# Performance work log

Hardware: AMD Instinct MI355X
Metric: run time of the kernel (lower is better)

The kernel has to match this reference:

```python
import jax, jax.numpy as jnp
import numpy as np

N_NODES = 40000
N_EDGES = 640000
D = 128  # in_channels == out_channels (required by the module's math)


def setup_inputs() -> dict:
    key = jax.random.key(0)
    ks = jax.random.split(key, 8)
    s = 1.0 / np.sqrt(D)  # torch Linear default init scale
    x = jax.random.normal(ks[0], (N_NODES, D), dtype=jnp.float32)
    edge_index = jax.random.randint(ks[1], (2, N_EDGES), 0, N_NODES, dtype=jnp.int64)
    Wn_w = jax.random.uniform(ks[2], (D, D), jnp.float32, -s, s)
    Wn_b = jax.random.uniform(ks[3], (D,), jnp.float32, -s, s)
    Wg_w = jax.random.uniform(ks[4], (D, D), jnp.float32, -s, s)
    Wg_b = jax.random.uniform(ks[5], (D,), jnp.float32, -s, s)
    Wa_w = jax.random.uniform(ks[6], (D, D), jnp.float32, -s, s)
    Wa_b = jax.random.uniform(ks[7], (D,), jnp.float32, -s, s)
    return {"x": x, "edge_index": edge_index,
            "Wn_w": Wn_w, "Wn_b": Wn_b,
            "Wg_w": Wg_w, "Wg_b": Wg_b,
            "Wa_w": Wa_w, "Wa_b": Wa_b}


def reference(x, edge_index, Wn_w, Wn_b, Wg_w, Wg_b, Wa_w, Wa_b):
    row, col = edge_index[0], edge_index[1]
    x_col = x[col]                                  # [E, D] gather
    alpha = jax.nn.sigmoid(x_col @ Wa_w + Wa_b)     # [E, D] edge attention
    neigh = x_col * alpha                           # [E, D]
    aggr = jax.ops.segment_sum(neigh, row, num_segments=x.shape[0])  # [N, D]
    out = jnp.tanh((x @ Wn_w + Wn_b) + (aggr @ Wg_w + Wg_b))
    return out  # dropout p=0.0 is identity
```

## Files before the change

### kernel.cpp

```cpp
#include <hip/hip_runtime.h>

#define NN 40000
#define NE 640000
#define D 128
#define CAP 64

typedef __attribute__((ext_vector_type(8))) short short8;
typedef __attribute__((ext_vector_type(4))) float f32x4;
typedef __attribute__((ext_vector_type(4))) int i32x4;

__device__ __forceinline__ short f2b(float v) {
  unsigned int u = __builtin_bit_cast(unsigned int, v);
  u = (u + 0x7fffu + ((u >> 16) & 1u)) >> 16;
  return (short)u;
}
__device__ __forceinline__ float b2f(short s) {
  unsigned int u = ((unsigned int)(unsigned short)s) << 16;
  return __builtin_bit_cast(float, u);
}

__global__ __launch_bounds__(256) void k_prep(
    const float* __restrict__ Wn, const float* __restrict__ Wg,
    const float* __restrict__ Wa, short* __restrict__ WnT,
    short* __restrict__ WgThi, short* __restrict__ WgTlo,
    short* __restrict__ WaT, int* __restrict__ cnt) {
  int i = blockIdx.x * 256 + threadIdx.x;
  int k = i >> 7, c = i & 127;
  WnT[c * D + k] = f2b(Wn[k * D + c]);
  WaT[c * D + k] = f2b(Wa[k * D + c]);
  float v = Wg[k * D + c];
  short hi = f2b(v);
  WgThi[c * D + k] = hi;
  WgTlo[c * D + k] = f2b(v - b2f(hi));
  if (i < 10000) {
    i32x4 z = {0, 0, 0, 0};
    *(i32x4*)(cnt + i * 4) = z;
  }
}

__global__ __launch_bounds__(256) void k_node(
    const float* __restrict__ x, const short* __restrict__ WaT,
    const short* __restrict__ WnT, const float* __restrict__ ba,
    float* __restrict__ xn_out, short* __restrict__ h_out) {
  int r0 = blockIdx.x * 16;
  int w = threadIdx.x >> 6, l = threadIdx.x & 63;
  int g = l >> 4, c16 = l & 15;
  int rowA = r0 + c16;

  short8 a[4];
#pragma unroll
  for (int kt = 0; kt < 4; ++kt) {
    const float* p = x + (size_t)rowA * D + kt * 32 + g * 8;
    f32x4 v0 = *(const f32x4*)p;
    f32x4 v1 = *(const f32x4*)(p + 4);
    short8 t;
    t[0] = f2b(v0[0]); t[1] = f2b(v0[1]); t[2] = f2b(v0[2]); t[3] = f2b(v0[3]);
    t[4] = f2b(v1[0]); t[5] = f2b(v1[1]); t[6] = f2b(v1[2]); t[7] = f2b(v1[3]);
    a[kt] = t;
  }

#pragma unroll
  for (int u = 0; u < 2; ++u) {
    int ct = w * 2 + u;
    int cc = ct * 16 + c16;
    f32x4 c = {0.f, 0.f, 0.f, 0.f};
#pragma unroll
    for (int kt = 0; kt < 4; ++kt) {
      short8 b = *(const short8*)(WaT + (size_t)cc * D + kt * 32 + g * 8);
      c = __builtin_amdgcn_mfma_f32_16x16x32_bf16(a[kt], b, c, 0, 0, 0);
    }
    float bav = ba[cc];
#pragma unroll
    for (int r = 0; r < 4; ++r) {
      int rr = r0 + g * 4 + r;
      float t = c[r] + bav;
      float al = 1.0f / (1.0f + __expf(-t));
      float xv = x[(size_t)rr * D + cc];
      h_out[(size_t)rr * D + cc] = f2b(xv * al);
    }
    f32x4 cn = {0.f, 0.f, 0.f, 0.f};
#pragma unroll
    for (int kt = 0; kt < 4; ++kt) {
      short8 b = *(const short8*)(WnT + (size_t)cc * D + kt * 32 + g * 8);
      cn = __builtin_amdgcn_mfma_f32_16x16x32_bf16(a[kt], b, cn, 0, 0, 0);
    }
#pragma unroll
    for (int r = 0; r < 4; ++r) {
      int rr = r0 + g * 4 + r;
      xn_out[(size_t)rr * D + cc] = cn[r];
    }
  }
}

__global__ __launch_bounds__(256) void k_fill(
    const int* __restrict__ ei, int* __restrict__ cnt,
    int* __restrict__ bucket) {
  int e = blockIdx.x * 256 + threadIdx.x;
  if (e >= NE) return;
  int r = ei[e];
  int c = ei[NE + e];
  int slot = atomicAdd(&cnt[r], 1);
  if (slot < CAP) bucket[r * CAP + slot] = c;
}

__global__ __launch_bounds__(256) void k_aggr(
    const int* __restrict__ cnt, const int* __restrict__ bucket,
    const short* __restrict__ h, float* __restrict__ s) {
  int l = threadIdx.x & 63;
  int n = blockIdx.x * 4 + (threadIdx.x >> 6);
  if (n >= NN) return;
  int g = l >> 4, i = l & 15;
  int deg = cnt[n];
  deg = deg < CAP ? deg : CAP;
  int bc = bucket[n * CAP + l];
  float acc[8];
#pragma unroll
  for (int q = 0; q < 8; ++q) acc[q] = 0.f;

  int j = 0;
  for (; j + 8 <= deg; j += 8) {
    int c0 = __shfl(bc, j + g);
    int c1 = __shfl(bc, j + 4 + g);
    short8 v0 = *(const short8*)(h + (size_t)c0 * D + i * 8);
    short8 v1 = *(const short8*)(h + (size_t)c1 * D + i * 8);
#pragma unroll
    for (int q = 0; q < 8; ++q) acc[q] += b2f(v0[q]);
#pragma unroll
    for (int q = 0; q < 8; ++q) acc[q] += b2f(v1[q]);
  }
  for (; j < deg; j += 4) {
    int src = j + g;
    int clamped = src < deg ? src : deg - 1;
    int c0 = __shfl(bc, clamped);
    if (src < deg) {
      short8 v0 = *(const short8*)(h + (size_t)c0 * D + i * 8);
#pragma unroll
      for (int q = 0; q < 8; ++q) acc[q] += b2f(v0[q]);
    }
  }

#pragma unroll
  for (int q = 0; q < 8; ++q) {
    acc[q] += __shfl_xor(acc[q], 16);
    acc[q] += __shfl_xor(acc[q], 32);
  }
  if (g == 0) {
    f32x4 lo = {acc[0], acc[1], acc[2], acc[3]};
    f32x4 hi = {acc[4], acc[5], acc[6], acc[7]};
    *(f32x4*)(s + (size_t)n * D + i * 8) = lo;
    *(f32x4*)(s + (size_t)n * D + i * 8 + 4) = hi;
  }
}

__global__ __launch_bounds__(256) void k_final(
    const float* __restrict__ s, const short* __restrict__ WgThi,
    const short* __restrict__ WgTlo, const float* __restrict__ bn,
    const float* __restrict__ bg, float* __restrict__ out) {
  int r0 = blockIdx.x * 16;
  int w = threadIdx.x >> 6, l = threadIdx.x & 63;
  int g = l >> 4, c16 = l & 15;
  int rowA = r0 + c16;

  short8 ahi[4], alo[4];
#pragma unroll
  for (int kt = 0; kt < 4; ++kt) {
    const float* p = s + (size_t)rowA * D + kt * 32 + g * 8;
    f32x4 v0 = *(const f32x4*)p;
    f32x4 v1 = *(const f32x4*)(p + 4);
    short8 hi, lo;
#pragma unroll
    for (int jq = 0; jq < 4; ++jq) {
      short hh = f2b(v0[jq]);
      hi[jq] = hh;
      lo[jq] = f2b(v0[jq] - b2f(hh));
    }
#pragma unroll
    for (int jq = 0; jq < 4; ++jq) {
      short hh = f2b(v1[jq]);
      hi[4 + jq] = hh;
      lo[4 + jq] = f2b(v1[jq] - b2f(hh));
    }
    ahi[kt] = hi;
    alo[kt] = lo;
  }

#pragma unroll
  for (int u = 0; u < 2; ++u) {
    int ct = w * 2 + u;
    int cc = ct * 16 + c16;
    f32x4 c = {0.f, 0.f, 0.f, 0.f};
#pragma unroll
    for (int kt = 0; kt < 4; ++kt) {
      short8 bh = *(const short8*)(WgThi + (size_t)cc * D + kt * 32 + g * 8);
      short8 bl = *(const short8*)(WgTlo + (size_t)cc * D + kt * 32 + g * 8);
      c = __builtin_amdgcn_mfma_f32_16x16x32_bf16(ahi[kt], bh, c, 0, 0, 0);
      c = __builtin_amdgcn_mfma_f32_16x16x32_bf16(alo[kt], bh, c, 0, 0, 0);
      c = __builtin_amdgcn_mfma_f32_16x16x32_bf16(ahi[kt], bl, c, 0, 0, 0);
    }
    float bias = bn[cc] + bg[cc];
#pragma unroll
    for (int r = 0; r < 4; ++r) {
      int rr = r0 + g * 4 + r;
      float z = c[r] + out[(size_t)rr * D + cc] + bias;
      out[(size_t)rr * D + cc] = tanhf(z);
    }
  }
}

extern "C" void kernel_launch(void* const* d_in, const int* in_sizes, int n_in,
                              void* d_out, int out_size, void* d_ws,
                              size_t ws_size, hipStream_t stream) {
  const float* x = (const float*)d_in[0];
  const int* ei = (const int*)d_in[1];
  const float* Wn_w = (const float*)d_in[2];
  const float* Wn_b = (const float*)d_in[3];
  const float* Wg_w = (const float*)d_in[4];
  const float* Wg_b = (const float*)d_in[5];
  const float* Wa_w = (const float*)d_in[6];
  const float* Wa_b = (const float*)d_in[7];

  char* ws = (char*)d_ws;
  short* WaT = (short*)(ws + 0);
  short* WnT = (short*)(ws + 32 * 1024);
  short* WgThi = (short*)(ws + 64 * 1024);
  short* WgTlo = (short*)(ws + 96 * 1024);
  int* cnt = (int*)(ws + 128 * 1024);
  float* s = (float*)(ws + 512 * 1024);
  short* h = (short*)(ws + 512 * 1024 + (size_t)NN * D * 4);
  int* bucket = (int*)(ws + 512 * 1024 + (size_t)NN * D * 6);
  float* out = (float*)d_out;

  k_prep<<<64, 256, 0, stream>>>(Wn_w, Wg_w, Wa_w, WnT, WgThi, WgTlo, WaT, cnt);
  k_node<<<NN / 16, 256, 0, stream>>>(x, WaT, WnT, Wa_b, out, h);
  k_fill<<<(NE + 255) / 256, 256, 0, stream>>>(ei, cnt, bucket);
  k_aggr<<<NN / 4, 256, 0, stream>>>(cnt, bucket, h, s);
  k_final<<<NN / 16, 256, 0, stream>>>(s, WgThi, WgTlo, Wn_b, Wg_b, out);
}
```

Before: 126.4 us.

## Move node linear into final kernel, stage tiles in LDS, compress bucket indices

The x@Wn product moves from k_node into k_final, so the intermediate fp32 result is no longer written to out and read back. k_node and k_final now stage x and s tiles through shared memory for coalesced loads, and h is written as vectorized short8 stores. Bucket indices become 16-bit and a zero sentinel row is added to h, so the aggregation loop runs branch-free in fixed 16-edge steps with padded gathers. The risks are extra redundant sentinel loads for low-degree nodes, and that 16-bit indices only hold because the node count fits in an unsigned short.

Result: faster. 111.3 us (-11.9%).

```diff
diff --git a/kernel.cpp b/kernel.cpp
--- a/kernel.cpp
+++ b/kernel.cpp
@@ -23,7 +23,7 @@
     const float* __restrict__ Wn, const float* __restrict__ Wg,
     const float* __restrict__ Wa, short* __restrict__ WnT,
     short* __restrict__ WgThi, short* __restrict__ WgTlo,
-    short* __restrict__ WaT, int* __restrict__ cnt) {
+    short* __restrict__ WaT, int* __restrict__ cnt, short* __restrict__ h) {
   int i = blockIdx.x * 256 + threadIdx.x;
   int k = i >> 7, c = i & 127;
   WnT[c * D + k] = f2b(Wn[k * D + c]);
@@ -36,75 +36,100 @@
     i32x4 z = {0, 0, 0, 0};
     *(i32x4*)(cnt + i * 4) = z;
   }
-}
-
-__global__ __launch_bounds__(256) void k_node(
-    const float* __restrict__ x, const short* __restrict__ WaT,
-    const short* __restrict__ WnT, const float* __restrict__ ba,
-    float* __restrict__ xn_out, short* __restrict__ h_out) {
-  int r0 = blockIdx.x * 16;
-  int w = threadIdx.x >> 6, l = threadIdx.x & 63;
-  int g = l >> 4, c16 = l & 15;
-  int rowA = r0 + c16;
-
-  short8 a[4];
-#pragma unroll
-  for (int kt = 0; kt < 4; ++kt) {
-    const float* p = x + (size_t)rowA * D + kt * 32 + g * 8;
-    f32x4 v0 = *(const f32x4*)p;
-    f32x4 v1 = *(const f32x4*)(p + 4);
-    short8 t;
-    t[0] = f2b(v0[0]); t[1] = f2b(v0[1]); t[2] = f2b(v0[2]); t[3] = f2b(v0[3]);
-    t[4] = f2b(v1[0]); t[5] = f2b(v1[1]); t[6] = f2b(v1[2]); t[7] = f2b(v1[3]);
-    a[kt] = t;
-  }
-
-#pragma unroll
-  for (int u = 0; u < 2; ++u) {
-    int ct = w * 2 + u;
-    int cc = ct * 16 + c16;
-    f32x4 c = {0.f, 0.f, 0.f, 0.f};
-#pragma unroll
-    for (int kt = 0; kt < 4; ++kt) {
-      short8 b = *(const short8*)(WaT + (size_t)cc * D + kt * 32 + g * 8);
-      c = __builtin_amdgcn_mfma_f32_16x16x32_bf16(a[kt], b, c, 0, 0, 0);
-    }
-    float bav = ba[cc];
-#pragma unroll
-    for (int r = 0; r < 4; ++r) {
-      int rr = r0 + g * 4 + r;
-      float t = c[r] + bav;
-      float al = 1.0f / (1.0f + __expf(-t));
-      float xv = x[(size_t)rr * D + cc];
-      h_out[(size_t)rr * D + cc] = f2b(xv * al);
-    }
-    f32x4 cn = {0.f, 0.f, 0.f, 0.f};
-#pragma unroll
-    for (int kt = 0; kt < 4; ++kt) {
-      short8 b = *(const short8*)(WnT + (size_t)cc * D + kt * 32 + g * 8);
-      cn = __builtin_amdgcn_mfma_f32_16x16x32_bf16(a[kt], b, cn, 0, 0, 0);
-    }
-#pragma unroll
-    for (int r = 0; r < 4; ++r) {
-      int rr = r0 + g * 4 + r;
-      xn_out[(size_t)rr * D + cc] = cn[r];
-    }
+  if (i < 16) {
+    short8 z = {0, 0, 0, 0, 0, 0, 0, 0};
+    *(short8*)(h + (size_t)NN * D + i * 8) = z;
   }
 }
 
 __global__ __launch_bounds__(256) void k_fill(
     const int* __restrict__ ei, int* __restrict__ cnt,
-    int* __restrict__ bucket) {
+    unsigned short* __restrict__ bucket) {
   int e = blockIdx.x * 256 + threadIdx.x;
   if (e >= NE) return;
   int r = ei[e];
   int c = ei[NE + e];
   int slot = atomicAdd(&cnt[r], 1);
-  if (slot < CAP) bucket[r * CAP + slot] = c;
-}
+  if (slot < CAP) bucket[(size_t)r * CAP + slot] = (unsigned short)c;
+}
+
+__global__ __launch_bounds__(256) void k_node(
+    const float* __restrict__ x, const short* __restrict__ WaT,
+    const float* __restrict__ ba, short* __restrict__ h_out) {
+  __shared__ float xs[16][132];
+  __shared__ float al_s[16][132];
+  int r0 = blockIdx.x * 16;
+  int t = threadIdx.x;
+  int w = t >> 6, l = t & 63;
+  int g = l >> 4, c16 = l & 15;
+
+#pragma unroll
+  for (int p = 0; p < 2; ++p) {
+    int idx = t + p * 256;
+    int row = idx >> 5, cv = idx & 31;
+    f32x4 v = *(const f32x4*)(x + (size_t)(r0 + row) * D + cv * 4);
+    *(f32x4*)&xs[row][cv * 4] = v;
+  }
+  __syncthreads();
+
+  short8 a[4];
+#pragma unroll
+  for (int kt = 0; kt < 4; ++kt) {
+    f32x4 v0 = *(const f32x4*)&xs[c16][kt * 32 + g * 8];
+    f32x4 v1 = *(const f32x4*)&xs[c16][kt * 32 + g * 8 + 4];
+    short8 tt;
+    tt[0] = f2b(v0[0]); tt[1] = f2b(v0[1]); tt[2] = f2b(v0[2]); tt[3] = f2b(v0[3]);
+    tt[4] = f2b(v1[0]); tt[5] = f2b(v1[1]); tt[6] = f2b(v1[2]); tt[7] = f2b(v1[3]);
+    a[kt] = tt;
+  }
+
+#pragma unroll
+  for (int u = 0; u < 2; ++u) {
+    int ct = w * 2 + u;
+    int cc = ct * 16 + c16;
+    f32x4 c = {0.f, 0.f, 0.f, 0.f};
+#pragma unroll
+    for (int kt = 0; kt < 4; ++kt) {
+      short8 b = *(const short8*)(WaT + (size_t)cc * D + kt * 32 + g * 8);
+      c = __builtin_amdgcn_mfma_f32_16x16x32_bf16(a[kt], b, c, 0, 0, 0);
+    }
+    float bav = ba[cc];
+#pragma unroll
+    for (int r = 0; r < 4; ++r) {
+      float tv = c[r] + bav;
+      al_s[g * 4 + r][cc] = 1.0f / (1.0f + __expf(-tv));
+    }
+  }
+  __syncthreads();
+
+  short8 hh;
+#pragma unroll
+  for (int q = 0; q < 8; ++q) {
+    float av = al_s[c16][w * 32 + g * 8 + q];
+    float xv = xs[c16][w * 32 + g * 8 + q];
+    hh[q] = f2b(xv * av);
+  }
+  *(short8*)(h_out + (size_t)(r0 + c16) * D + w * 32 + g * 8) = hh;
+}
+
+#define SSTEP(S0, CA, CB, CC, CD)                                   \
+  {                                                                 \
+    int q0 = (S0) + g < deg ? (CA) : NN;                            \
+    int q1 = (S0) + 4 + g < deg ? (CB) : NN;                        \
+    int q2 = (S0) + 8 + g < deg ? (CC) : NN;                        \
+    int q3 = (S0) + 12 + g < deg ? (CD) : NN;                       \
+    short8 v0 = *(const short8*)(h + (size_t)q0 * D + i * 8);       \
+    short8 v1 = *(const short8*)(h + (size_t)q1 * D + i * 8);       \
+    short8 v2 = *(const short8*)(h + (size_t)q2 * D + i * 8);       \
+    short8 v3 = *(const short8*)(h + (size_t)q3 * D + i * 8);       \
+    _Pragma("unroll") for (int q = 0; q < 8; ++q) {                 \
+      acc[q] += b2f(v0[q]) + b2f(v1[q]);                            \
+      acc[q] += b2f(v2[q]) + b2f(v3[q]);                            \
+    }                                                               \
+  }
 
 __global__ __launch_bounds__(256) void k_aggr(
-    const int* __restrict__ cnt, const int* __restrict__ bucket,
+    const int* __restrict__ cnt, const unsigned short* __restrict__ bucket,
     const short* __restrict__ h, float* __restrict__ s) {
   int l = threadIdx.x & 63;
   int n = blockIdx.x * 4 + (threadIdx.x >> 6);
@@ -112,30 +137,24 @@
   int g = l >> 4, i = l & 15;
   int deg = cnt[n];
   deg = deg < CAP ? deg : CAP;
-  int bc = bucket[n * CAP + l];
+  int bc = bucket[(size_t)n * CAP + l];
   float acc[8];
 #pragma unroll
   for (int q = 0; q < 8; ++q) acc[q] = 0.f;
 
-  int j = 0;
-  for (; j + 8 <= deg; j += 8) {
-    int c0 = __shfl(bc, j + g);
-    int c1 = __shfl(bc, j + 4 + g);
-    short8 v0 = *(const short8*)(h + (size_t)c0 * D + i * 8);
-    short8 v1 = *(const short8*)(h + (size_t)c1 * D + i * 8);
-#pragma unroll
-    for (int q = 0; q < 8; ++q) acc[q] += b2f(v0[q]);
-#pragma unroll
-    for (int q = 0; q < 8; ++q) acc[q] += b2f(v1[q]);
-  }
-  for (; j < deg; j += 4) {
-    int src = j + g;
-    int clamped = src < deg ? src : deg - 1;
-    int c0 = __shfl(bc, clamped);
-    if (src < deg) {
-      short8 v0 = *(const short8*)(h + (size_t)c0 * D + i * 8);
-#pragma unroll
-      for (int q = 0; q < 8; ++q) acc[q] += b2f(v0[q]);
+  int c0 = __shfl(bc, g), c1 = __shfl(bc, 4 + g);
+  int c2 = __shfl(bc, 8 + g), c3 = __shfl(bc, 12 + g);
+  SSTEP(0, c0, c1, c2, c3);
+  if (deg > 16) {
+    int c4 = __shfl(bc, 16 + g), c5 = __shfl(bc, 20 + g);
+    int c6 = __shfl(bc, 24 + g), c7 = __shfl(bc, 28 + g);
+    SSTEP(16, c4, c5, c6, c7);
+  }
+  if (deg > 32) {
+    for (int j = 32; j < deg; j += 16) {
+      int d0 = __shfl(bc, (j + g) & 63), d1 = __shfl(bc, (j + 4 + g) & 63);
+      int d2 = __shfl(bc, (j + 8 + g) & 63), d3 = __shfl(bc, (j + 12 + g) & 63);
+      SSTEP(j, d0, d1, d2, d3);
     }
   }
 
@@ -153,35 +172,54 @@
 }
 
 __global__ __launch_bounds__(256) void k_final(
-    const float* __restrict__ s, const short* __restrict__ WgThi,
+    const float* __restrict__ x, const float* __restrict__ s,
+    const short* __restrict__ WnT, const short* __restrict__ WgThi,
     const short* __restrict__ WgTlo, const float* __restrict__ bn,
     const float* __restrict__ bg, float* __restrict__ out) {
+  __shared__ float xs[16][132];
+  __shared__ float ss[16][132];
   int r0 = blockIdx.x * 16;
-  int w = threadIdx.x >> 6, l = threadIdx.x & 63;
+  int t = threadIdx.x;
+  int w = t >> 6, l = t & 63;
   int g = l >> 4, c16 = l & 15;
-  int rowA = r0 + c16;
-
-  short8 ahi[4], alo[4];
+
+#pragma unroll
+  for (int p = 0; p < 2; ++p) {
+    int idx = t + p * 256;
+    int row = idx >> 5, cv = idx & 31;
+    *(f32x4*)&xs[row][cv * 4] =
+        *(const f32x4*)(x + (size_t)(r0 + row) * D + cv * 4);
+    *(f32x4*)&ss[row][cv * 4] =
+        *(const f32x4*)(s + (size_t)(r0 + row) * D + cv * 4);
+  }
+  __syncthreads();
+
+  short8 axf[4], sh[4], sl[4];
 #pragma unroll
   for (int kt = 0; kt < 4; ++kt) {
-    const float* p = s + (size_t)rowA * D + kt * 32 + g * 8;
-    f32x4 v0 = *(const f32x4*)p;
-    f32x4 v1 = *(const f32x4*)(p + 4);
-    short8 hi, lo;
+    f32x4 xv0 = *(const f32x4*)&xs[c16][kt * 32 + g * 8];
+    f32x4 xv1 = *(const f32x4*)&xs[c16][kt * 32 + g * 8 + 4];
+    short8 tx;
+    tx[0] = f2b(xv0[0]); tx[1] = f2b(xv0[1]); tx[2] = f2b(xv0[2]); tx[3] = f2b(xv0[3]);
+    tx[4] = f2b(xv1[0]); tx[5] = f2b(xv1[1]); tx[6] = f2b(xv1[2]); tx[7] = f2b(xv1[3]);
+    axf[kt] = tx;
+    f32x4 sv0 = *(const f32x4*)&ss[c16][kt * 32 + g * 8];
+    f32x4 sv1 = *(const f32x4*)&ss[c16][kt * 32 + g * 8 + 4];
+    short8 th, tl;
 #pragma unroll
     for (int jq = 0; jq < 4; ++jq) {
-      short hh = f2b(v0[jq]);
-      hi[jq] = hh;
-      lo[jq] = f2b(v0[jq] - b2f(hh));
+      short hh = f2b(sv0[jq]);
+      th[jq] = hh;
+      tl[jq] = f2b(sv0[jq] - b2f(hh));
     }
 #pragma unroll
     for (int jq = 0; jq < 4; ++jq) {
-      short hh = f2b(v1[jq]);
-      hi[4 + jq] = hh;
-      lo[4 + jq] = f2b(v1[jq] - b2f(hh));
-    }
-    ahi[kt] = hi;
-    alo[kt] = lo;
+      short hh = f2b(sv1[jq]);
+      th[4 + jq] = hh;
+      tl[4 + jq] = f2b(sv1[jq] - b2f(hh));
+    }
+    sh[kt] = th;
+    sl[kt] = tl;
   }
 
 #pragma unroll
@@ -191,18 +229,19 @@
     f32x4 c = {0.f, 0.f, 0.f, 0.f};
 #pragma unroll
     for (int kt = 0; kt < 4; ++kt) {
+      short8 bwn = *(const short8*)(WnT + (size_t)cc * D + kt * 32 + g * 8);
       short8 bh = *(const short8*)(WgThi + (size_t)cc * D + kt * 32 + g * 8);
       short8 bl = *(const short8*)(WgTlo + (size_t)cc * D + kt * 32 + g * 8);
-      c = __builtin_amdgcn_mfma_f32_16x16x32_bf16(ahi[kt], bh, c, 0, 0, 0);
-      c = __builtin_amdgcn_mfma_f32_16x16x32_bf16(alo[kt], bh, c, 0, 0, 0);
-      c = __builtin_amdgcn_mfma_f32_16x16x32_bf16(ahi[kt], bl, c, 0, 0, 0);
+      c = __builtin_amdgcn_mfma_f32_16x16x32_bf16(axf[kt], bwn, c, 0, 0, 0);
+      c = __builtin_amdgcn_mfma_f32_16x16x32_bf16(sh[kt], bh, c, 0, 0, 0);
+      c = __builtin_amdgcn_mfma_f32_16x16x32_bf16(sl[kt], bh, c, 0, 0, 0);
+      c = __builtin_amdgcn_mfma_f32_16x16x32_bf16(sh[kt], bl, c, 0, 0, 0);
     }
     float bias = bn[cc] + bg[cc];
 #pragma unroll
     for (int r = 0; r < 4; ++r) {
       int rr = r0 + g * 4 + r;
-      float z = c[r] + out[(size_t)rr * D + cc] + bias;
-      out[(size_t)rr * D + cc] = tanhf(z);
+      out[(size_t)rr * D + cc] = tanhf(c[r] + bias);
     }
   }
 }
@@ -225,14 +264,19 @@
   short* WgThi = (short*)(ws + 64 * 1024);
   short* WgTlo = (short*)(ws + 96 * 1024);
   int* cnt = (int*)(ws + 128 * 1024);
-  float* s = (float*)(ws + 512 * 1024);
-  short* h = (short*)(ws + 512 * 1024 + (size_t)NN * D * 4);
-  int* bucket = (int*)(ws + 512 * 1024 + (size_t)NN * D * 6);
+  size_t off = 512 * 1024;
+  short* h = (short*)(ws + off);
+  off += (size_t)(NN + 1) * D * 2;
+  unsigned short* bucket = (unsigned short*)(ws + off);
+  off += (size_t)NN * CAP * 2;
+  float* s = (float*)(ws + off);
   float* out = (float*)d_out;
 
-  k_prep<<<64, 256, 0, stream>>>(Wn_w, Wg_w, Wa_w, WnT, WgThi, WgTlo, WaT, cnt);
-  k_node<<<NN / 16, 256, 0, stream>>>(x, WaT, WnT, Wa_b, out, h);
+  k_prep<<<64, 256, 0, stream>>>(Wn_w, Wg_w, Wa_w, WnT, WgThi, WgTlo, WaT,
+                                 cnt, h);
   k_fill<<<(NE + 255) / 256, 256, 0, stream>>>(ei, cnt, bucket);
+  k_node<<<NN / 16, 256, 0, stream>>>(x, WaT, Wa_b, h);
   k_aggr<<<NN / 4, 256, 0, stream>>>(cnt, bucket, h, s);
-  k_final<<<NN / 16, 256, 0, stream>>>(s, WgThi, WgTlo, Wn_b, Wg_b, out);
-}
+  k_final<<<NN / 16, 256, 0, stream>>>(x, s, WnT, WgThi, WgTlo, Wn_b, Wg_b,
+                                       out);
+}
```
